# Kernel optimization log

Hardware: AMD Instinct MI355X
Metric: run time of the kernel (lower is better)

Reference implementation:

```python
import jax, jax.numpy as jnp
import numpy as np

B, N, E, H, HEADS = 4, 10000, 160000, 128, 4
NEG_SLOPE = 0.2  # PyG GATConv default
LN_EPS = 1e-5


def setup_inputs() -> dict:
    key = jax.random.key(0)
    ks = jax.random.split(key, 24)
    inp = {}
    inp["node_embeddings"] = jax.random.normal(ks[0], (B, N, H), dtype=jnp.float32)
    inp["src_index"] = jax.random.randint(ks[1], (B, E), 0, N)
    inp["tgt_index"] = jax.random.randint(ks[2], (B, E), 0, N)
    sc = 1.0 / np.sqrt(H)
    for i in range(3):
        j = 3 + 3 * i
        inp[f"W{i+1}"] = jax.random.normal(ks[j], (H, HEADS * H), dtype=jnp.float32) * sc
        inp[f"att_src{i+1}"] = jax.random.normal(ks[j + 1], (HEADS, H), dtype=jnp.float32) * sc
        inp[f"att_dst{i+1}"] = jax.random.normal(ks[j + 2], (HEADS, H), dtype=jnp.float32) * sc
        inp[f"bias{i+1}"] = jnp.zeros((H,), dtype=jnp.float32)
    inp["ln1_g"] = jnp.ones((H,), dtype=jnp.float32)
    inp["ln1_b"] = jnp.zeros((H,), dtype=jnp.float32)
    inp["ln2_g"] = jnp.ones((H,), dtype=jnp.float32)
    inp["ln2_b"] = jnp.zeros((H,), dtype=jnp.float32)
    return inp


def _layer_norm(x, g, b):
    mu = jnp.mean(x, axis=-1, keepdims=True)
    var = jnp.mean((x - mu) ** 2, axis=-1, keepdims=True)
    return (x - mu) * jax.lax.rsqrt(var + LN_EPS) * g + b


def _gat(x, src, tgt, W, a_s, a_d, b):
    # x: [N, H]; src/tgt: [E'] (self-loops already appended). eval mode -> no dropout.
    h = (x @ W).reshape(N, HEADS, H)               # [N, heads, H]
    e_src = jnp.einsum('nhc,hc->nh', h, a_s)       # [N, heads]
    e_dst = jnp.einsum('nhc,hc->nh', h, a_d)
    e = jax.nn.leaky_relu(e_src[src] + e_dst[tgt], NEG_SLOPE)  # [E', heads]
    m = jax.ops.segment_max(e, tgt, num_segments=N)            # per-target max
    ex = jnp.exp(e - m[tgt])
    s = jax.ops.segment_sum(ex, tgt, num_segments=N)
    alpha = ex / s[tgt]                                        # [E', heads]
    out = jax.ops.segment_sum(alpha[:, :, None] * h[src], tgt, num_segments=N)
    return out.mean(axis=1) + b                                # concat=False -> head mean


def reference(node_embeddings, src_index, tgt_index,
              W1, att_src1, att_dst1, bias1,
              W2, att_src2, att_dst2, bias2,
              W3, att_src3, att_dst3, bias3,
              ln1_g, ln1_b, ln2_g, ln2_b):
    loop = jnp.arange(N, dtype=src_index.dtype)

    def one_graph(x, src, tgt):
        s = jnp.concatenate([src, loop])   # GATConv add_self_loops=True (default)
        t = jnp.concatenate([tgt, loop])
        m = _gat(x, s, t, W1, att_src1, att_dst1, bias1)
        m = jax.nn.relu(_layer_norm(m, ln1_g, ln1_b))
        m = _gat(m, s, t, W2, att_src2, att_dst2, bias2)
        m = jax.nn.relu(_layer_norm(m, ln2_g, ln2_b))
        m = _gat(m, s, t, W3, att_src3, att_dst3, bias3)
        return m

    return jax.vmap(one_graph)(node_embeddings, src_index, tgt_index)
```

## Files before the change

### kernel.cpp

```cpp
#include <hip/hip_runtime.h>
#include <hip/hip_bf16.h>
#include <cstdint>
#include <cstddef>

#define B_ 4
#define N_ 10000
#define E_ 160000
#define H_ 128
#define HEADS_ 4
#define HH_ 512
#define NROWS (B_*N_)

typedef __attribute__((ext_vector_type(8))) short bf16x8;
typedef __attribute__((ext_vector_type(4))) float f32x4;
typedef __attribute__((ext_vector_type(2))) float f32x2;

__device__ __forceinline__ float lrelu(float x){ return x > 0.f ? x : 0.2f*x; }
__device__ __forceinline__ unsigned short f2b(float f){
  unsigned int u = __builtin_bit_cast(unsigned int, f);
  unsigned int r = (u + 0x7fffu + ((u >> 16) & 1u)) >> 16;
  return (unsigned short)r;
}
__device__ __forceinline__ float blo(unsigned int u){ return __builtin_bit_cast(float, u << 16); }
__device__ __forceinline__ float bhi(unsigned int u){ return __builtin_bit_cast(float, u & 0xffff0000u); }

__device__ __forceinline__ void acc_row(f32x2* ac, float al, uint4 h){
  f32x2 v = {al, al};
  ac[0] += v * (f32x2){blo(h.x), bhi(h.x)};
  ac[1] += v * (f32x2){blo(h.y), bhi(h.y)};
  ac[2] += v * (f32x2){blo(h.z), bhi(h.z)};
  ac[3] += v * (f32x2){blo(h.w), bhi(h.w)};
}

__global__ void k_count(const int* __restrict__ tgt, int* __restrict__ cnt){
  int e = blockIdx.x*blockDim.x + threadIdx.x;
  int b = blockIdx.y;
  int t = tgt[(size_t)b*E_ + e];
  atomicAdd(&cnt[b*N_ + t], 1);
}

__global__ void k_scan(const int* __restrict__ cnt, int* __restrict__ off, int* __restrict__ cursor){
  int b = blockIdx.x;
  __shared__ int wsum[16];
  __shared__ int carry_s;
  int lane = threadIdx.x & 63, wid = threadIdx.x >> 6;
  if (threadIdx.x == 0){ carry_s = 0; off[b*(N_+1)] = 0; }
  __syncthreads();
  for (int base = 0; base < N_; base += 1024){
    int i = base + threadIdx.x;
    int v = (i < N_) ? cnt[b*N_ + i] : 0;
    int x = v;
    #pragma unroll
    for (int d = 1; d < 64; d <<= 1){
      int y = __shfl_up(x, d);
      if (lane >= d) x += y;
    }
    if (lane == 63) wsum[wid] = x;
    __syncthreads();
    if (wid == 0 && lane < 16){
      int w = wsum[lane];
      #pragma unroll
      for (int d = 1; d < 16; d <<= 1){
        int y = __shfl_up(w, d, 16);
        if (lane >= d) w += y;
      }
      wsum[lane] = w;
    }
    __syncthreads();
    int excl = (wid ? wsum[wid-1] : 0) + carry_s;
    if (i < N_){
      int inc = x + excl;
      off[b*(N_+1) + i + 1] = inc;
      cursor[b*N_ + i] = inc - v;
    }
    __syncthreads();
    if (threadIdx.x == 0) carry_s += wsum[15];
    __syncthreads();
  }
}

__global__ void k_scatter(const int* __restrict__ src, const int* __restrict__ tgt,
                          int* __restrict__ cursor, int* __restrict__ csr){
  int e = blockIdx.x*blockDim.x + threadIdx.x;
  int b = blockIdx.y;
  int t = tgt[(size_t)b*E_ + e];
  int pos = atomicAdd(&cursor[b*N_ + t], 1);
  csr[(size_t)b*E_ + pos] = src[(size_t)b*E_ + e];
}

__global__ void k_prep(const float* __restrict__ W0, const float* __restrict__ W1, const float* __restrict__ W2,
                       const float* __restrict__ as0, const float* __restrict__ as1, const float* __restrict__ as2,
                       const float* __restrict__ ad0, const float* __restrict__ ad1, const float* __restrict__ ad2,
                       float* __restrict__ wasA, float* __restrict__ wadA, unsigned short* __restrict__ wtA){
  int l = blockIdx.y;
  const float* W   = (l==0)?W0:(l==1)?W1:W2;
  const float* asp = (l==0)?as0:(l==1)?as1:as2;
  const float* adp = (l==0)?ad0:(l==1)?ad1:ad2;
  if (blockIdx.x < 256){
    int i = blockIdx.x*256 + threadIdx.x;
    int c = i >> 7, k = i & 127;
    wtA[(size_t)l*HH_*H_ + i] = f2b(W[(size_t)k*HH_ + c]);
  } else {
    int j = (blockIdx.x - 256)*256 + threadIdx.x;
    if (j < H_*HEADS_){
      int k = j >> 2, h = j & 3;
      const float* wrow = W + (size_t)k*HH_ + h*H_;
      const float* asr = asp + h*H_;
      const float* adr = adp + h*H_;
      float ss = 0.f, sd = 0.f;
      for (int c = 0; c < H_; ++c){ float w = wrow[c]; ss += w*asr[c]; sd += w*adr[c]; }
      wasA[l*HH_ + j] = ss; wadA[l*HH_ + j] = sd;
    }
  }
}

__global__ __launch_bounds__(256) void k_cast_logits(const float* __restrict__ X,
    const float* __restrict__ was, const float* __restrict__ wad,
    unsigned short* __restrict__ Xb, float* __restrict__ es, float* __restrict__ ed){
  int gw = (blockIdx.x*blockDim.x + threadIdx.x) >> 6;
  int lane = threadIdx.x & 63;
  float2 v = *(const float2*)(X + (size_t)gw*H_ + lane*2);
  unsigned int o = ((unsigned int)f2b(v.y) << 16) | (unsigned int)f2b(v.x);
  *(unsigned int*)(Xb + (size_t)gw*H_ + lane*2) = o;
  int c = lane*2;
  const f32x4* w4 = (const f32x4*)was;
  const f32x4* d4 = (const f32x4*)wad;
  f32x4 se = v.x*w4[c] + v.y*w4[c+1];
  f32x4 de = v.x*d4[c] + v.y*d4[c+1];
  #pragma unroll
  for (int d = 1; d < 64; d <<= 1){
    se.x += __shfl_xor(se.x,d); se.y += __shfl_xor(se.y,d);
    se.z += __shfl_xor(se.z,d); se.w += __shfl_xor(se.w,d);
    de.x += __shfl_xor(de.x,d); de.y += __shfl_xor(de.y,d);
    de.z += __shfl_xor(de.z,d); de.w += __shfl_xor(de.w,d);
  }
  if (lane == 0){
    *(float4*)(es + (size_t)gw*4) = make_float4(se.x, se.y, se.z, se.w);
    *(float4*)(ed + (size_t)gw*4) = make_float4(de.x, de.y, de.z, de.w);
  }
}

__global__ __launch_bounds__(256) void k_gemm_mfma(const unsigned short* __restrict__ Xb,
    const unsigned short* __restrict__ Wt, unsigned short* __restrict__ Hb){
  __shared__ unsigned short xs[64*128];
  __shared__ unsigned short ws[64*128];
  int row0 = blockIdx.x * 64, col0 = blockIdx.y * 64;
  int tid = threadIdx.x;
  int ch = tid & 15, r0 = tid >> 4;
  #pragma unroll
  for (int p = 0; p < 4; ++p){
    int r = r0 + p*16;
    int sc = ch ^ (r & 7);
    *(uint4*)(&xs[r*128 + sc*8]) = *(const uint4*)(Xb + (size_t)(row0 + r)*H_ + ch*8);
    *(uint4*)(&ws[r*128 + sc*8]) = *(const uint4*)(Wt + (size_t)(col0 + r)*H_ + ch*8);
  }
  __syncthreads();
  int w = tid >> 6, l = tid & 63;
  int lr = l & 15, q = l >> 4;
  f32x4 z = {0.f, 0.f, 0.f, 0.f};
  f32x4 acc[4] = {z, z, z, z};
  int arow = w*16 + lr;
  #pragma unroll
  for (int kf = 0; kf < 4; ++kf){
    int bch = kf*4 + q;
    bf16x8 a = *(const bf16x8*)(&xs[arow*128 + (bch ^ (arow & 7))*8]);
    #pragma unroll
    for (int cf = 0; cf < 4; ++cf){
      int brow = cf*16 + lr;
      bf16x8 bfr = *(const bf16x8*)(&ws[brow*128 + (bch ^ (brow & 7))*8]);
      acc[cf] = __builtin_amdgcn_mfma_f32_16x16x32_bf16(a, bfr, acc[cf], 0, 0, 0);
    }
  }
  #pragma unroll
  for (int cf = 0; cf < 4; ++cf){
    #pragma unroll
    for (int rg = 0; rg < 4; ++rg){
      int row = row0 + w*16 + q*4 + rg;
      int col = col0 + cf*16 + lr;
      Hb[(size_t)row*HH_ + col] = f2b(acc[cf][rg]);
    }
  }
}

template<bool FINAL>
__global__ __launch_bounds__(256, 4) void k_aggregate(
    const unsigned short* __restrict__ Hb,
    const float* __restrict__ es, const float* __restrict__ ed,
    const int* __restrict__ off, const int* __restrict__ csr,
    const float* __restrict__ bias,
    const float* __restrict__ wasN, const float* __restrict__ wadN,
    const float* __restrict__ lng, const float* __restrict__ lnb,
    float* __restrict__ Yout, unsigned short* __restrict__ Xbout,
    float* __restrict__ esN, float* __restrict__ edN)
{
  __shared__ float alpha_s[4][4][68];
  __shared__ int   srcn_s[4][64];
  __shared__ float orow_s[4][128];
  int wv = threadIdx.x >> 6, lane = threadIdx.x & 63;
  int gw = blockIdx.x*4 + wv;
  int b = gw / N_, t = gw - b*N_;
  const float4 edv = *(const float4*)(ed + (size_t)gw*4);
  int start = off[b*(N_+1) + t];
  int deg = off[b*(N_+1) + t + 1] - start;
  int total = deg + 1;
  const int* lst = csr + (size_t)b*E_ + start;
  const float* esb = es + (size_t)b*N_*4;
  int head = lane >> 4;
  int cb = head*H_ + (lane & 15)*8;
  const unsigned short* hbase = Hb + (size_t)b*N_*HH_;
  f32x2 zz = {0.f, 0.f};
  f32x2 ac[4] = {zz, zz, zz, zz};

  if (total <= 64){
    bool valid = lane < total;
    int srcn = (lane < deg) ? lst[lane] : t;
    srcn_s[wv][lane] = srcn;
    float4 ev = *(const float4*)(esb + (size_t)srcn*4);
    __builtin_amdgcn_wave_barrier();
    int4 s0 = *(const int4*)(&srcn_s[wv][0]);
    int4 s1 = *(const int4*)(&srcn_s[wv][4]);
    uint4 g0 = *(const uint4*)(hbase + (size_t)s0.x*HH_ + cb);
    uint4 g1 = *(const uint4*)(hbase + (size_t)s0.y*HH_ + cb);
    uint4 g2 = *(const uint4*)(hbase + (size_t)s0.z*HH_ + cb);
    uint4 g3 = *(const uint4*)(hbase + (size_t)s0.w*HH_ + cb);
    uint4 g4 = *(const uint4*)(hbase + (size_t)s1.x*HH_ + cb);
    uint4 g5 = *(const uint4*)(hbase + (size_t)s1.y*HH_ + cb);
    uint4 g6 = *(const uint4*)(hbase + (size_t)s1.z*HH_ + cb);
    uint4 g7 = *(const uint4*)(hbase + (size_t)s1.w*HH_ + cb);

    float e0 = valid ? lrelu(ev.x + edv.x) : -1e30f;
    float e1 = valid ? lrelu(ev.y + edv.y) : -1e30f;
    float e2 = valid ? lrelu(ev.z + edv.z) : -1e30f;
    float e3 = valid ? lrelu(ev.w + edv.w) : -1e30f;
    float M0 = e0, M1 = e1, M2 = e2, M3 = e3;
    #pragma unroll
    for (int d = 1; d < 64; d <<= 1){
      M0 = fmaxf(M0, __shfl_xor(M0, d)); M1 = fmaxf(M1, __shfl_xor(M1, d));
      M2 = fmaxf(M2, __shfl_xor(M2, d)); M3 = fmaxf(M3, __shfl_xor(M3, d));
    }
    float p0 = valid ? __expf(e0 - M0) : 0.f;
    float p1 = valid ? __expf(e1 - M1) : 0.f;
    float p2 = valid ? __expf(e2 - M2) : 0.f;
    float p3 = valid ? __expf(e3 - M3) : 0.f;
    float S0 = p0, S1 = p1, S2 = p2, S3 = p3;
    #pragma unroll
    for (int d = 1; d < 64; d <<= 1){
      S0 += __shfl_xor(S0, d); S1 += __shfl_xor(S1, d);
      S2 += __shfl_xor(S2, d); S3 += __shfl_xor(S3, d);
    }
    alpha_s[wv][0][lane] = p0/S0;
    alpha_s[wv][1][lane] = p1/S1;
    alpha_s[wv][2][lane] = p2/S2;
    alpha_s[wv][3][lane] = p3/S3;
    __builtin_amdgcn_wave_barrier();

    const float* alp = &alpha_s[wv][head][0];
    const int*   srp = &srcn_s[wv][0];
    {
      float4 al0 = *(const float4*)(alp);
      float4 al1 = *(const float4*)(alp + 4);
      acc_row(ac, al0.x, g0); acc_row(ac, al0.y, g1);
      acc_row(ac, al0.z, g2); acc_row(ac, al0.w, g3);
      acc_row(ac, al1.x, g4); acc_row(ac, al1.y, g5);
      acc_row(ac, al1.z, g6); acc_row(ac, al1.w, g7);
    }
    int nc = (total + 7) >> 3;
    for (int ck = 1; ck < nc; ++ck){
      int base = ck*8;
      float4 al0 = *(const float4*)(alp + base);
      float4 al1 = *(const float4*)(alp + base + 4);
      int4 c0 = *(const int4*)(srp + base);
      int4 c1 = *(const int4*)(srp + base + 4);
      uint4 h0 = *(const uint4*)(hbase + (size_t)c0.x*HH_ + cb);
      uint4 h1 = *(const uint4*)(hbase + (size_t)c0.y*HH_ + cb);
      uint4 h2 = *(const uint4*)(hbase + (size_t)c0.z*HH_ + cb);
      uint4 h3 = *(const uint4*)(hbase + (size_t)c0.w*HH_ + cb);
      uint4 h4 = *(const uint4*)(hbase + (size_t)c1.x*HH_ + cb);
      uint4 h5 = *(const uint4*)(hbase + (size_t)c1.y*HH_ + cb);
      uint4 h6 = *(const uint4*)(hbase + (size_t)c1.z*HH_ + cb);
      uint4 h7 = *(const uint4*)(hbase + (size_t)c1.w*HH_ + cb);
      acc_row(ac, al0.x, h0); acc_row(ac, al0.y, h1);
      acc_row(ac, al0.z, h2); acc_row(ac, al0.w, h3);
      acc_row(ac, al1.x, h4); acc_row(ac, al1.y, h5);
      acc_row(ac, al1.z, h6); acc_row(ac, al1.w, h7);
    }
  } else {
    float m0=-1e30f, m1=-1e30f, m2=-1e30f, m3=-1e30f;
    float s0=0.f, s1=0.f, s2=0.f, s3=0.f;
    for (int i2 = lane; i2 <= deg; i2 += 64){
      int srcn = (i2 < deg) ? lst[i2] : t;
      float4 ev = *(const float4*)(esb + (size_t)srcn*4);
      float e0 = lrelu(ev.x + edv.x);
      float e1 = lrelu(ev.y + edv.y);
      float e2 = lrelu(ev.z + edv.z);
      float e3 = lrelu(ev.w + edv.w);
      float nm;
      nm = fmaxf(m0, e0); s0 = s0*__expf(m0-nm) + __expf(e0-nm); m0 = nm;
      nm = fmaxf(m1, e1); s1 = s1*__expf(m1-nm) + __expf(e1-nm); m1 = nm;
      nm = fmaxf(m2, e2); s2 = s2*__expf(m2-nm) + __expf(e2-nm); m2 = nm;
      nm = fmaxf(m3, e3); s3 = s3*__expf(m3-nm) + __expf(e3-nm); m3 = nm;
    }
    #pragma unroll
    for (int d = 1; d < 64; d <<= 1){
      float om, os, nm;
      om = __shfl_xor(m0, d); os = __shfl_xor(s0, d); nm = fmaxf(m0, om);
      s0 = s0*__expf(m0-nm) + os*__expf(om-nm); m0 = nm;
      om = __shfl_xor(m1, d); os = __shfl_xor(s1, d); nm = fmaxf(m1, om);
      s1 = s1*__expf(m1-nm) + os*__expf(om-nm); m1 = nm;
      om = __shfl_xor(m2, d); os = __shfl_xor(s2, d); nm = fmaxf(m2, om);
      s2 = s2*__expf(m2-nm) + os*__expf(om-nm); m2 = nm;
      om = __shfl_xor(m3, d); os = __shfl_xor(s3, d); nm = fmaxf(m3, om);
      s3 = s3*__expf(m3-nm) + os*__expf(om-nm); m3 = nm;
    }
    float mh, sh, edh;
    if      (head == 0){ mh = m0; sh = s0; edh = edv.x; }
    else if (head == 1){ mh = m1; sh = s1; edh = edv.y; }
    else if (head == 2){ mh = m2; sh = s2; edh = edv.z; }
    else               { mh = m3; sh = s3; edh = edv.w; }
    float rh = 1.0f / sh;
    for (int i2 = 0; i2 < total; ++i2){
      int srcn = (i2 < deg) ? lst[i2] : t;
      float eh = esb[(size_t)srcn*4 + head];
      float al = __expf(lrelu(eh + edh) - mh) * rh;
      uint4 hA = *(const uint4*)(hbase + (size_t)srcn*HH_ + cb);
      acc_row(ac, al, hA);
    }
  }

  float a[8] = {ac[0].x, ac[0].y, ac[1].x, ac[1].y, ac[2].x, ac[2].y, ac[3].x, ac[3].y};
  #pragma unroll
  for (int d = 16; d < 64; d <<= 1)
    #pragma unroll
    for (int j = 0; j < 8; j++) a[j] += __shfl_xor(a[j], d);

  int c = (lane & 15)*8;
  if (FINAL){
    if (lane < 16){
      float4 o0 = make_float4(0.25f*a[0]+bias[c+0], 0.25f*a[1]+bias[c+1],
                              0.25f*a[2]+bias[c+2], 0.25f*a[3]+bias[c+3]);
      float4 o1 = make_float4(0.25f*a[4]+bias[c+4], 0.25f*a[5]+bias[c+5],
                              0.25f*a[6]+bias[c+6], 0.25f*a[7]+bias[c+7]);
      *(float4*)(Yout + (size_t)gw*H_ + c)     = o0;
      *(float4*)(Yout + (size_t)gw*H_ + c + 4) = o1;
    }
  } else {
    float o[8];
    #pragma unroll
    for (int j = 0; j < 8; j++) o[j] = 0.25f*a[j] + bias[c+j];
    float ss = 0.f;
    #pragma unroll
    for (int j = 0; j < 8; j++) ss += o[j];
    #pragma unroll
    for (int d = 1; d < 16; d <<= 1) ss += __shfl_xor(ss, d);
    float mu = ss * (1.f/H_);
    float vv = 0.f;
    #pragma unroll
    for (int j = 0; j < 8; j++){ float dx = o[j]-mu; vv += dx*dx; }
    #pragma unroll
    for (int d = 1; d < 16; d <<= 1) vv += __shfl_xor(vv, d);
    float inv = rsqrtf(vv*(1.f/H_) + 1e-5f);
    float4 g0 = *(const float4*)(lng + c), g1 = *(const float4*)(lng + c + 4);
    float4 b0 = *(const float4*)(lnb + c), b1 = *(const float4*)(lnb + c + 4);
    float gg[8] = {g0.x,g0.y,g0.z,g0.w,g1.x,g1.y,g1.z,g1.w};
    float bb[8] = {b0.x,b0.y,b0.z,b0.w,b1.x,b1.y,b1.z,b1.w};
    float oo[8];
    #pragma unroll
    for (int j = 0; j < 8; j++) oo[j] = fmaxf((o[j]-mu)*inv*gg[j] + bb[j], 0.f);
    if (lane < 16){
      uint4 up;
      up.x = ((unsigned int)f2b(oo[1]) << 16) | f2b(oo[0]);
      up.y = ((unsigned int)f2b(oo[3]) << 16) | f2b(oo[2]);
      up.z = ((unsigned int)f2b(oo[5]) << 16) | f2b(oo[4]);
      up.w = ((unsigned int)f2b(oo[7]) << 16) | f2b(oo[6]);
      *(uint4*)(Xbout + (size_t)gw*H_ + lane*8) = up;
      *(float4*)(&orow_s[wv][c])     = make_float4(oo[0], oo[1], oo[2], oo[3]);
      *(float4*)(&orow_s[wv][c + 4]) = make_float4(oo[4], oo[5], oo[6], oo[7]);
    }
    __builtin_amdgcn_wave_barrier();
    float pe = 0.f, pd = 0.f;
    #pragma unroll
    for (int j = 0; j < 8; j++){
      float xv = orow_s[wv][c + j];
      pe += xv * wasN[(c + j)*4 + head];
      pd += xv * wadN[(c + j)*4 + head];
    }
    #pragma unroll
    for (int d = 1; d < 16; d <<= 1){ pe += __shfl_xor(pe, d); pd += __shfl_xor(pd, d); }
    if ((lane & 15) == 0){
      esN[(size_t)gw*4 + head] = pe;
      edN[(size_t)gw*4 + head] = pd;
    }
  }
}

extern "C" void kernel_launch(void* const* d_in, const int* in_sizes, int n_in,
                              void* d_out, int out_size, void* d_ws, size_t ws_size,
                              hipStream_t stream){
  const float* x0   = (const float*)d_in[0];
  const int*   srcI = (const int*)d_in[1];
  const int*   tgtI = (const int*)d_in[2];
  const float* Wl[3]  = {(const float*)d_in[3], (const float*)d_in[7],  (const float*)d_in[11]};
  const float* asl[3] = {(const float*)d_in[4], (const float*)d_in[8],  (const float*)d_in[12]};
  const float* adl[3] = {(const float*)d_in[5], (const float*)d_in[9],  (const float*)d_in[13]};
  const float* bl[3]  = {(const float*)d_in[6], (const float*)d_in[10], (const float*)d_in[14]};
  const float* lng[2] = {(const float*)d_in[15], (const float*)d_in[17]};
  const float* lnb[2] = {(const float*)d_in[16], (const float*)d_in[18]};

  char* p = (char*)d_ws;
  auto carve = [&](size_t bytes) -> void* {
    void* r = (void*)p; p += (bytes + 255) & ~(size_t)255; return r;
  };
  int*   off    = (int*)carve((size_t)B_*(N_+1)*4);
  int*   cnt    = (int*)carve((size_t)B_*N_*4);
  int*   cursor = (int*)carve((size_t)B_*N_*4);
  int*   csr    = (int*)carve((size_t)B_*E_*4);
  float* es2[2] = {(float*)carve((size_t)NROWS*4*4), (float*)carve((size_t)NROWS*4*4)};
  float* ed2[2] = {(float*)carve((size_t)NROWS*4*4), (float*)carve((size_t)NROWS*4*4)};
  float* wasA   = (float*)carve((size_t)3*HH_*4);
  float* wadA   = (float*)carve((size_t)3*HH_*4);
  unsigned short* wtA  = (unsigned short*)carve((size_t)3*HH_*H_*2);
  unsigned short* hbuf = (unsigned short*)carve((size_t)NROWS*HH_*2);
  unsigned short* xbf  = (unsigned short*)carve((size_t)NROWS*H_*2);

  hipMemsetAsync(cnt, 0, (size_t)B_*N_*4, stream);
  k_count  <<<dim3(E_/256, B_), 256, 0, stream>>>(tgtI, cnt);
  k_scan   <<<B_, 1024, 0, stream>>>(cnt, off, cursor);
  k_scatter<<<dim3(E_/256, B_), 256, 0, stream>>>(srcI, tgtI, cursor, csr);
  k_prep   <<<dim3(258, 3), 256, 0, stream>>>(Wl[0], Wl[1], Wl[2],
                                              asl[0], asl[1], asl[2],
                                              adl[0], adl[1], adl[2],
                                              wasA, wadA, wtA);
  k_cast_logits<<<NROWS/4, 256, 0, stream>>>(x0, wasA, wadA, xbf, es2[0], ed2[0]);

  for (int l = 0; l < 3; ++l){
    k_gemm_mfma<<<dim3(NROWS/64, HH_/64), 256, 0, stream>>>(xbf, wtA + (size_t)l*HH_*H_, hbuf);
    int cur = l & 1, nxt = cur ^ 1;
    if (l < 2){
      k_aggregate<false><<<NROWS/4, 256, 0, stream>>>(hbuf, es2[cur], ed2[cur], off, csr, bl[l],
          wasA + (size_t)(l+1)*HH_, wadA + (size_t)(l+1)*HH_, lng[l], lnb[l],
          nullptr, xbf, es2[nxt], ed2[nxt]);
    } else {
      k_aggregate<true><<<NROWS/4, 256, 0, stream>>>(hbuf, es2[cur], ed2[cur], off, csr, bl[l],
          nullptr, nullptr, nullptr, nullptr,
          (float*)d_out, nullptr, nullptr, nullptr);
    }
  }
}
```

Baseline: 473.0 us.

## Stream neighbor row gathers through LDS with an 8-deep async pipeline

In the small-degree path of the aggregation kernel, per-lane register gathers of neighbor feature rows are replaced by global_load_lds transfers into a per-wave ring buffer of 8 rows. The wave issues up to 8 row loads ahead, then consumes one row per iteration after waiting on vmcnt and immediately refills that slot, using sched_barrier to keep ordering. The goal is to keep more gather traffic in flight and overlap it with the softmax computation. In exchange it adds 32 KB of LDS per block, which may lower occupancy, and it issues one explicit memory wait per neighbor.

```diff
diff --git a/kernel.cpp b/kernel.cpp
--- a/kernel.cpp
+++ b/kernel.cpp
@@ -10,10 +10,14 @@
 #define HEADS_ 4
 #define HH_ 512
 #define NROWS (B_*N_)
+#define DEPTH 8
 
 typedef __attribute__((ext_vector_type(8))) short bf16x8;
 typedef __attribute__((ext_vector_type(4))) float f32x4;
 typedef __attribute__((ext_vector_type(2))) float f32x2;
+
+#define SB() __builtin_amdgcn_sched_barrier(0)
+#define WAITV(N) do { asm volatile("s_waitcnt vmcnt(" #N ")" ::: "memory"); __builtin_amdgcn_sched_barrier(0); } while(0)
 
 __device__ __forceinline__ float lrelu(float x){ return x > 0.f ? x : 0.2f*x; }
 __device__ __forceinline__ unsigned short f2b(float f){
@@ -30,6 +34,12 @@
   ac[1] += v * (f32x2){blo(h.y), bhi(h.y)};
   ac[2] += v * (f32x2){blo(h.z), bhi(h.z)};
   ac[3] += v * (f32x2){blo(h.w), bhi(h.w)};
+}
+
+__device__ __forceinline__ void issue_gather(const unsigned short* hrow, unsigned short* slot, int lane){
+  __builtin_amdgcn_global_load_lds(
+      (const __attribute__((address_space(1))) void*)(hrow + lane*8),
+      (__attribute__((address_space(3))) void*)slot, 16, 0, 0);
 }
 
 __global__ void k_count(const int* __restrict__ tgt, int* __restrict__ cnt){
@@ -193,6 +203,7 @@
     float* __restrict__ Yout, unsigned short* __restrict__ Xbout,
     float* __restrict__ esN, float* __restrict__ edN)
 {
+  __shared__ unsigned short gbuf[4][DEPTH][HH_];
   __shared__ float alpha_s[4][4][68];
   __shared__ int   srcn_s[4][64];
   __shared__ float orow_s[4][128];
@@ -217,16 +228,13 @@
     srcn_s[wv][lane] = srcn;
     float4 ev = *(const float4*)(esb + (size_t)srcn*4);
     __builtin_amdgcn_wave_barrier();
-    int4 s0 = *(const int4*)(&srcn_s[wv][0]);
-    int4 s1 = *(const int4*)(&srcn_s[wv][4]);
-    uint4 g0 = *(const uint4*)(hbase + (size_t)s0.x*HH_ + cb);
-    uint4 g1 = *(const uint4*)(hbase + (size_t)s0.y*HH_ + cb);
-    uint4 g2 = *(const uint4*)(hbase + (size_t)s0.z*HH_ + cb);
-    uint4 g3 = *(const uint4*)(hbase + (size_t)s0.w*HH_ + cb);
-    uint4 g4 = *(const uint4*)(hbase + (size_t)s1.x*HH_ + cb);
-    uint4 g5 = *(const uint4*)(hbase + (size_t)s1.y*HH_ + cb);
-    uint4 g6 = *(const uint4*)(hbase + (size_t)s1.z*HH_ + cb);
-    uint4 g7 = *(const uint4*)(hbase + (size_t)s1.w*HH_ + cb);
+    const int* srp = &srcn_s[wv][0];
+
+    asm volatile("s_waitcnt vmcnt(0)" ::: "memory"); SB();
+    int nIssue = total < DEPTH ? total : DEPTH;
+    for (int s = 0; s < nIssue; ++s)
+      issue_gather(hbase + (size_t)srp[s]*HH_, &gbuf[wv][s][0], lane);
+    SB();
 
     float e0 = valid ? lrelu(ev.x + edv.x) : -1e30f;
     float e1 = valid ? lrelu(ev.y + edv.y) : -1e30f;
@@ -253,36 +261,24 @@
     alpha_s[wv][2][lane] = p2/S2;
     alpha_s[wv][3][lane] = p3/S3;
     __builtin_amdgcn_wave_barrier();
-
     const float* alp = &alpha_s[wv][head][0];
-    const int*   srp = &srcn_s[wv][0];
-    {
-      float4 al0 = *(const float4*)(alp);
-      float4 al1 = *(const float4*)(alp + 4);
-      acc_row(ac, al0.x, g0); acc_row(ac, al0.y, g1);
-      acc_row(ac, al0.z, g2); acc_row(ac, al0.w, g3);
-      acc_row(ac, al1.x, g4); acc_row(ac, al1.y, g5);
-      acc_row(ac, al1.z, g6); acc_row(ac, al1.w, g7);
-    }
-    int nc = (total + 7) >> 3;
-    for (int ck = 1; ck < nc; ++ck){
-      int base = ck*8;
-      float4 al0 = *(const float4*)(alp + base);
-      float4 al1 = *(const float4*)(alp + base + 4);
-      int4 c0 = *(const int4*)(srp + base);
-      int4 c1 = *(const int4*)(srp + base + 4);
-      uint4 h0 = *(const uint4*)(hbase + (size_t)c0.x*HH_ + cb);
-      uint4 h1 = *(const uint4*)(hbase + (size_t)c0.y*HH_ + cb);
-      uint4 h2 = *(const uint4*)(hbase + (size_t)c0.z*HH_ + cb);
-      uint4 h3 = *(const uint4*)(hbase + (size_t)c0.w*HH_ + cb);
-      uint4 h4 = *(const uint4*)(hbase + (size_t)c1.x*HH_ + cb);
-      uint4 h5 = *(const uint4*)(hbase + (size_t)c1.y*HH_ + cb);
-      uint4 h6 = *(const uint4*)(hbase + (size_t)c1.z*HH_ + cb);
-      uint4 h7 = *(const uint4*)(hbase + (size_t)c1.w*HH_ + cb);
-      acc_row(ac, al0.x, h0); acc_row(ac, al0.y, h1);
-      acc_row(ac, al0.z, h2); acc_row(ac, al0.w, h3);
-      acc_row(ac, al1.x, h4); acc_row(ac, al1.y, h5);
-      acc_row(ac, al1.z, h6); acc_row(ac, al1.w, h7);
+    int lane8 = lane*8;
+
+    int i = 0;
+    for (; i + DEPTH < total; ++i){
+      WAITV(7);
+      float al = alp[i];
+      uint4 hA = *(const uint4*)(&gbuf[wv][i & (DEPTH-1)][lane8]);
+      acc_row(ac, al, hA);
+      SB();
+      issue_gather(hbase + (size_t)srp[i + DEPTH]*HH_, &gbuf[wv][i & (DEPTH-1)][0], lane);
+      SB();
+    }
+    asm volatile("s_waitcnt vmcnt(0)" ::: "memory"); SB();
+    for (; i < total; ++i){
+      float al = alp[i];
+      uint4 hA = *(const uint4*)(&gbuf[wv][i & (DEPTH-1)][lane8]);
+      acc_row(ac, al, hA);
     }
   } else {
     float m0=-1e30f, m1=-1e30f, m2=-1e30f, m3=-1e30f;
```

Result: slower. 524.8 us (+11.0%).
